# Performance work log

Measured on AMD Instinct MI355X. Metric: run time of the kernel, lower is better.

The kernel has to match this reference:

```python
import jax, jax.numpy as jnp
import numpy as np

# Hyperparameters from init_kwargs
K = 1024           # num_embeddings
D = 256            # embedding_dim
COMMIT = 0.25      # commitment_cost
DECAY = 0.99
LAMBDA = 1e-05
NU = 0.1
TAU = 0.5


def setup_inputs() -> dict:
    key = jax.random.key(0)
    k1, k2, k3 = jax.random.split(key, 3)
    B, H, W = 32, 32, 32
    N = B * H * W
    inputs = jax.random.normal(k1, (B, D, H, W), jnp.float32)
    weight = jax.random.normal(k2, (K, D), jnp.float32) * 0.02  # codebook
    # EMA buffers as initialized on first training step (non-kmeans branch)
    ema_count = jnp.full((K,), N / K, jnp.float32)
    ema_weight = weight * ema_count[:, None]
    # Gumbel noise used by F.gumbel_softmax(-distances, tau, hard=True)
    gumbel_noise = jax.random.gumbel(k3, (N, K), jnp.float32)
    return {"inputs": inputs, "weight": weight, "ema_count": ema_count,
            "ema_weight": ema_weight, "gumbel_noise": gumbel_noise}


def reference(inputs, weight, ema_count, ema_weight, gumbel_noise):
    B, C, H, W = inputs.shape
    # b d h w -> (b h w) d
    x = jnp.transpose(inputs, (0, 2, 3, 1)).reshape(-1, C)  # [N, D]
    N = x.shape[0]

    distances = (jnp.sum(x * x, axis=1, keepdims=True)
                 + jnp.sum(weight * weight, axis=1)
                 - 2.0 * jnp.einsum('nd,kd->nk', x, weight))

    soft_encodings = jax.nn.softmax(-distances / TAU, axis=-1)  # [N, K]

    # Hard gumbel-softmax sample (computed under no_grad in torch):
    # argmax((logits + g)/tau) == argmax(logits + g), logits = -distances
    idx = jnp.argmax(-distances + gumbel_noise, axis=-1)        # [N]
    encodings = jax.nn.one_hot(idx, K, dtype=x.dtype)           # [N, K]

    quantized = (encodings @ weight).reshape(B, H, W, C)        # [B,H,W,D]

    # EMA codebook update (training branch, no_grad)
    new_count = ema_count * DECAY + jnp.sum(soft_encodings, axis=0) * (1.0 - DECAY)
    new_count = (new_count + LAMBDA) / (N + K * LAMBDA) * N
    d_weight = jnp.einsum('nk,nd->kd', soft_encodings, x)
    new_ema_weight = ema_weight * DECAY + d_weight * (1.0 - DECAY)
    new_embedding = new_ema_weight / new_count[:, None]

    # Negative-entropy commitment loss on soft assignments
    probs = soft_encodings
    loss_latents = jnp.mean(jnp.sum(probs * jnp.log(jnp.clip(probs, 1e-08)), axis=-1))
    loss = COMMIT * loss_latents

    # quantized + nu*(quantized - detach(quantized)) == quantized in value
    quantized = quantized + NU * (quantized - jax.lax.stop_gradient(quantized))

    avg_probs = jnp.mean(encodings, axis=0)
    perplexity = jnp.exp(-jnp.sum(avg_probs * jnp.log(avg_probs + 1e-10)))

    quantized_out = jnp.transpose(quantized, (0, 3, 1, 2))  # [B,D,H,W]
    return (loss, quantized_out, perplexity, encodings,
            new_count, new_ema_weight, new_embedding)
```

## Files before the change

kernel.cpp:

```cpp
#include <hip/hip_runtime.h>
#include <math.h>

#define NROWS 32768
#define KCB   1024
#define DDIM  256
#define NHALF 16384

#define O_LOSS 0
#define O_Q    1
#define O_PERP 8388609
#define O_ENC  8388610
#define O_NCNT 41943042
#define O_EMAW 41944066
#define O_EMB  42206210

#define E_XS3   2
#define E_S     12582914

#define W_WSQ  0
#define W_XSQ  1024
#define W_IDX  33792
#define W_COL  66560
#define W_HCNT 67584
#define W_BENT 68608
#define W_NCNT 76800
#define W_T2I  77824
#define W_WB   143360
#define W_MROW 274432
#define W_IROW 307200

typedef __attribute__((ext_vector_type(8))) short bf16x8;
typedef __attribute__((ext_vector_type(4))) float f32x4;

#define GLOAD_LDS16(g, l) __builtin_amdgcn_global_load_lds( \
    (const __attribute__((address_space(1))) unsigned int*)(g), \
    (__attribute__((address_space(3))) unsigned int*)(l), 16, 0, 0)

__device__ __forceinline__ float wred_sum(float v) {
#pragma unroll
  for (int off = 32; off > 0; off >>= 1) v += __shfl_xor(v, off);
  return v;
}
__device__ __forceinline__ ushort f2bf(float f) {
  union { float f; unsigned u; } c; c.f = f;
  unsigned u = c.u;
  return (ushort)((u + 0x7fffu + ((u >> 16) & 1u)) >> 16);
}
__device__ __forceinline__ float bf2f(ushort h) {
  union { unsigned u; float f; } c; c.u = ((unsigned)h) << 16;
  return c.f;
}

__global__ void k_init(float* __restrict__ hcnt) {
  int i = blockIdx.x * 256 + threadIdx.x;
  if (i < 1024) hcnt[i] = 0.f;
}

__global__ void k_wsplit(const float* __restrict__ w, float* __restrict__ wsq,
                         ushort* __restrict__ WB) {
  int t = threadIdx.x;
  int lane = t & 63, wv = t >> 6;
  int k = blockIdx.x * 4 + wv;
  int d0 = lane * 4;
  float4 v = *(const float4*)&w[(size_t)k * DDIM + d0];
  float s = v.x * v.x + v.y * v.y + v.z * v.z + v.w * v.w;
  s = wred_sum(s);
  if (lane == 0) wsq[k] = s;
  float vv[4] = {v.x, v.y, v.z, v.w};
  union { ushort u[4]; uint2 q; } hh;
#pragma unroll
  for (int q = 0; q < 4; ++q) hh.u[q] = f2bf(vv[q]);
  *(uint2*)&WB[(size_t)k * 256 + d0] = hh.q;
}

__global__ __launch_bounds__(256) void k_xsplit(const float* __restrict__ x,
                                                ushort* __restrict__ XS3,
                                                float* __restrict__ xsq) {
  __shared__ __align__(16) ushort sl[32 * 776];
  __shared__ float sq[32 * 9];
  int t = threadIdx.x;
  int b = blockIdx.x >> 5, mt = blockIdx.x & 31;
  int m0 = mt * 32, mloc = t & 31, dgrp = t >> 5;
  const float* xb = x + (size_t)b * DDIM * 1024 + m0 + mloc;
  float s = 0.f;
#pragma unroll
  for (int jj = 0; jj < 8; ++jj) {
    int d0 = dgrp * 32 + jj * 4;
    float vv[4];
#pragma unroll
    for (int q = 0; q < 4; ++q) vv[q] = xb[(size_t)(d0 + q) * 1024];
    union { ushort u[4]; uint2 q; } hh, mi, lo;
#pragma unroll
    for (int q = 0; q < 4; ++q) {
      float v = vv[q];
      ushort h = f2bf(v);
      float r1 = v - bf2f(h);
      ushort m_ = f2bf(r1);
      float r2 = r1 - bf2f(m_);
      hh.u[q] = h; mi.u[q] = m_; lo.u[q] = f2bf(r2);
      s = fmaf(v, v, s);
    }
    int base = mloc * 776;
    *(uint2*)&sl[base + d0] = hh.q;
    *(uint2*)&sl[base + 256 + d0] = mi.q;
    *(uint2*)&sl[base + 512 + d0] = lo.q;
  }
  sq[mloc * 9 + dgrp] = s;
  __syncthreads();
  if (t < 32) {
    float ss = 0.f;
#pragma unroll
    for (int gq = 0; gq < 8; ++gq) ss += sq[t * 9 + gq];
    xsq[b * 1024 + m0 + t] = ss;
  }
  ushort* dst = XS3 + (size_t)(b * 1024 + m0) * 768;
#pragma unroll
  for (int p = 0; p < 12; ++p) {
    int idx = p * 256 + t;
    int row = idx / 96;
    int co = idx - row * 96;
    *(uint4*)&dst[(size_t)row * 768 + co * 8] = *(uint4*)&sl[row * 776 + co * 8];
  }
}

__global__ __launch_bounds__(256) void k_gemm1t(const ushort* __restrict__ XS3h,
                                                const ushort* __restrict__ WB,
                                                const float* __restrict__ wsq,
                                                const float* __restrict__ xsqh,
                                                float* __restrict__ S) {
  __shared__ __align__(16) ushort Asl[2][8192];
  __shared__ __align__(16) ushort Bsl[2][8192];
  __shared__ float xsl[128];
  __shared__ float wsl[128];
  int t = threadIdx.x;
  int h = blockIdx.x;
  int xcd = h & 7, seq = h >> 3;
  int kt = seq & 7;
  int nt = xcd * 16 + (seq >> 3);
  int n0 = nt * 128;
  int k0 = kt * 128;
  int l = t & 63, wid = t >> 6;
  int wr = wid >> 1, wc = wid & 1;
  int hi = l >> 4, c = l & 15;

  if (t < 128) { xsl[t] = xsqh[n0 + t]; wsl[t] = wsq[k0 + t]; }

  f32x4 zero = {0.f, 0.f, 0.f, 0.f};
  f32x4 acc[4][4];
#pragma unroll
  for (int i = 0; i < 4; ++i)
#pragma unroll
    for (int j = 0; j < 4; ++j) acc[i][j] = zero;

  const char* XSb = (const char*)XS3h;
  const char* WBb = (const char*)WB;
  int lr = l >> 3;
  int lsw = ((l & 7) ^ lr) << 4;

#define STAGE(s_, b_)                                                              \
  {                                                                                \
    size_t bofs_ = (size_t)((s_) & 3) << 7;                                        \
    size_t aofs_ = ((s_) < 4) ? ((size_t)(s_) << 7)                                \
                              : (size_t)(512 + (((s_) - 4) << 7));                 \
    char* Ad_ = (char*)Asl + (b_) * 16384;                                         \
    char* Bd_ = (char*)Bsl + (b_) * 16384;                                         \
    _Pragma("unroll")                                                              \
    for (int q_ = 0; q_ < 4; ++q_) {                                               \
      int seg_ = wid * 32 + q_ * 8;                                                \
      GLOAD_LDS16(XSb + (size_t)(n0 + seg_ + lr) * 1536 + aofs_ + lsw,             \
                  Ad_ + seg_ * 128);                                               \
      GLOAD_LDS16(WBb + (size_t)(k0 + seg_ + lr) * 512 + bofs_ + lsw,              \
                  Bd_ + seg_ * 128);                                               \
    }                                                                              \
  }

  STAGE(0, 0);
  asm volatile("s_waitcnt vmcnt(0)" ::: "memory");
  __builtin_amdgcn_s_barrier();
  __builtin_amdgcn_sched_barrier(0);

  int buf = 0;
  for (int s = 0; s < 8; ++s) {
    if (s < 7) STAGE(s + 1, buf ^ 1);
    const ushort* Ab = &Asl[buf][0];
    const ushort* Bb = &Bsl[buf][0];
#pragma unroll
    for (int kk = 0; kk < 2; ++kk) {
      bf16x8 af[4], bg[4];
#pragma unroll
      for (int i = 0; i < 4; ++i) {
        int row = wr * 64 + i * 16 + c;
        int ch = (kk * 4 + hi) ^ (row & 7);
        af[i] = *(const bf16x8*)&Ab[row * 64 + ch * 8];
      }
#pragma unroll
      for (int j = 0; j < 4; ++j) {
        int row = wc * 64 + j * 16 + c;
        int ch = (kk * 4 + hi) ^ (row & 7);
        bg[j] = *(const bf16x8*)&Bb[row * 64 + ch * 8];
      }
#pragma unroll
      for (int i = 0; i < 4; ++i)
#pragma unroll
        for (int j = 0; j < 4; ++j)
          acc[i][j] = __builtin_amdgcn_mfma_f32_16x16x32_bf16(af[i], bg[j], acc[i][j], 0, 0, 0);
    }
    asm volatile("s_waitcnt vmcnt(0)" ::: "memory");
    __builtin_amdgcn_s_barrier();
    buf ^= 1;
  }
#undef STAGE

#pragma unroll
  for (int i = 0; i < 4; ++i) {
#pragma unroll
    for (int r = 0; r < 4; ++r) {
      int nl = wr * 64 + i * 16 + hi * 4 + r;
      float xs = xsl[nl];
#pragma unroll
      for (int j = 0; j < 4; ++j) {
        int kl = wc * 64 + j * 16 + c;
        float nd = fmaf(2.f, acc[i][j][r], -(xs + wsl[kl]));
        S[(size_t)(n0 + nl) * 1024 + k0 + kl] = nd;
      }
    }
  }
}

__global__ __launch_bounds__(256) void k_rowstat(const float* __restrict__ S,
                                                 const float* __restrict__ Gh,
                                                 float* __restrict__ Mrowh,
                                                 float* __restrict__ Irowh,
                                                 float* __restrict__ benth,
                                                 int* __restrict__ t2igh) {
  __shared__ float went[4];
  int t = threadIdx.x;
  int l = t & 63, wv = t >> 6;
  int n = blockIdx.x * 4 + wv;
  const float* row = S + ((size_t)n << 10);
  const float* grow = Gh + ((size_t)n << 10);
  float v[16];
  float mx = -3.0e38f;
  float v1 = -3.0e38f, v2 = -3.0e38f;
  int i1 = 0x7fffffff, i2 = 0x7fffffff;
#pragma unroll
  for (int j = 0; j < 4; ++j) {
    float4 a = *(const float4*)&row[j * 256 + l * 4];
    float4 gg = *(const float4*)&grow[j * 256 + l * 4];
    float av[4] = {a.x, a.y, a.z, a.w};
    float gv[4] = {gg.x, gg.y, gg.z, gg.w};
#pragma unroll
    for (int q = 0; q < 4; ++q) {
      v[j * 4 + q] = av[q];
      mx = fmaxf(mx, av[q]);
      float sc = av[q] + gv[q];
      int kk = j * 256 + l * 4 + q;
      if (sc > v1 || (sc == v1 && kk < i1)) { v2 = v1; i2 = i1; v1 = sc; i1 = kk; }
      else if (sc > v2 || (sc == v2 && kk < i2)) { v2 = sc; i2 = kk; }
    }
  }
#pragma unroll
  for (int off = 1; off < 64; off <<= 1) {
    mx = fmaxf(mx, __shfl_xor(mx, off));
    float ov1 = __shfl_xor(v1, off), ov2 = __shfl_xor(v2, off);
    int oi1 = __shfl_xor(i1, off), oi2 = __shfl_xor(i2, off);
    bool fB = (ov1 > v1) || (ov1 == v1 && oi1 < i1);
    float nv1 = fB ? ov1 : v1; int ni1 = fB ? oi1 : i1;
    float ca = fB ? v1 : ov1;  int cia = fB ? i1 : oi1;
    float cb = fB ? ov2 : v2;  int cib = fB ? oi2 : i2;
    bool sB = (cb > ca) || (cb == ca && cib < cia);
    v1 = nv1; i1 = ni1;
    v2 = sB ? cb : ca; i2 = sB ? cib : cia;
  }
  float M = 2.f * mx;
  float e[16]; float ps = 0.f;
#pragma unroll
  for (int u = 0; u < 16; ++u) { e[u] = __expf(fmaf(2.f, v[u], -M)); ps += e[u]; }
  ps = wred_sum(ps);
  float inv = 1.f / ps;
  float ent = 0.f;
#pragma unroll
  for (int u = 0; u < 16; ++u) {
    float sfv = e[u] * inv;
    ent += sfv * __logf(fmaxf(sfv, 1e-8f));
  }
  ent = wred_sum(ent);
  if (l == 0) {
    t2igh[n * 2] = i1; t2igh[n * 2 + 1] = i2;
    Mrowh[n] = M; Irowh[n] = inv;
    went[wv] = ent;
  }
  __syncthreads();
  if (t == 0) benth[blockIdx.x] = went[0] + went[1] + went[2] + went[3];
}

__global__ __launch_bounds__(512) void k_rowwrite(const float* __restrict__ S,
                                                  const float* __restrict__ Mrowh,
                                                  const float* __restrict__ Irowh,
                                                  ushort* __restrict__ sTp) {
  __shared__ ushort lds[64 * 65];
  __shared__ float Ml[64], Il[64];
  int t = threadIdx.x;
  int n0 = blockIdx.x * 64;
  if (t < 64) { Ml[t] = Mrowh[n0 + t]; Il[t] = Irowh[n0 + t]; }
  __syncthreads();
  for (int kt = 0; kt < 16; ++kt) {
    int k0 = kt * 64;
    int row = t >> 3, c8 = (t & 7) * 8;
    float M = Ml[row], inv = Il[row];
    const float* sp = &S[(size_t)(n0 + row) * 1024 + k0 + c8];
    float4 a = *(const float4*)sp;
    float4 b = *(const float4*)(sp + 4);
    float sv[8] = {a.x, a.y, a.z, a.w, b.x, b.y, b.z, b.w};
    ushort* d = &lds[row * 65 + c8];
#pragma unroll
    for (int j = 0; j < 8; ++j)
      d[j] = f2bf(__expf(fmaf(2.f, sv[j], -M)) * inv);
    __syncthreads();
    int krow = t >> 3, nc8 = (t & 7) * 8;
    uint* dst = (uint*)&sTp[(size_t)(k0 + krow) * NHALF + n0 + nc8];
#pragma unroll
    for (int j = 0; j < 4; ++j) {
      uint lo = lds[(nc8 + 2 * j) * 65 + krow];
      uint hh = lds[(nc8 + 2 * j + 1) * 65 + krow];
      dst[j] = lo | (hh << 16);
    }
    __syncthreads();
  }
}

__global__ __launch_bounds__(256) void k_refine(const ushort* __restrict__ XS3,
                                                const float* __restrict__ w,
                                                const float* __restrict__ wsq,
                                                const float* __restrict__ xsq,
                                                const float* __restrict__ G,
                                                const int* __restrict__ t2ig,
                                                int* __restrict__ idxArr,
                                                float* __restrict__ hcnt) {
  int t = threadIdx.x;
  int l = t & 63, wv = t >> 6;
  int base = blockIdx.x * 64 + wv * 16;
  int d0 = l * 4;
  for (int rr = 0; rr < 16; ++rr) {
    int n = base + rr;
    const ushort* p = XS3 + (size_t)n * 768;
    union { uint2 q; ushort u[4]; } ha, ma, la;
    ha.q = *(const uint2*)&p[d0];
    ma.q = *(const uint2*)&p[256 + d0];
    la.q = *(const uint2*)&p[512 + d0];
    float xv[4];
#pragma unroll
    for (int q = 0; q < 4; ++q) xv[q] = bf2f(ha.u[q]) + bf2f(ma.u[q]) + bf2f(la.u[q]);
    float xs = xsq[n];
    int ia = t2ig[n * 2], ib = t2ig[n * 2 + 1];
    float sc[2];
    int ids[2] = {ia, ib};
#pragma unroll
    for (int cdd = 0; cdd < 2; ++cdd) {
      int id = ids[cdd];
      const float* wr = w + (size_t)id * DDIM;
      float4 wv4 = *(const float4*)&wr[d0];
      float d = xv[0] * wv4.x + xv[1] * wv4.y + xv[2] * wv4.z + xv[3] * wv4.w;
      d = wred_sum(d);
      sc[cdd] = fmaf(2.f, d, -xs) - wsq[id] + G[((size_t)n << 10) + id];
    }
    int win = (sc[1] > sc[0] || (sc[1] == sc[0] && ib < ia)) ? ib : ia;
    if (l == 0) {
      idxArr[n] = win;
      atomicAdd(&hcnt[win], 1.f);
    }
  }
}

__global__ void k_quant(const float* __restrict__ w, const int* __restrict__ idxArr,
                        float* __restrict__ outQ) {
  int n = blockIdx.x * 256 + threadIdx.x;
  int b = n >> 10, m = n & 1023;
  int id = idxArr[n];
  const float* wr = w + (size_t)id * DDIM;
  float* o = outQ + (size_t)b * DDIM * 1024 + m;
#pragma unroll 4
  for (int d = 0; d < DDIM; ++d) o[(size_t)d * 1024] = wr[d];
}

__global__ __launch_bounds__(512) void k_gemm2_mfma(const ushort* __restrict__ sT0,
                                                    const ushort* __restrict__ sT1,
                                                    const float* __restrict__ x,
                                                    float* __restrict__ P) {
  __shared__ __align__(16) ushort Abuf[256 * 72];
  __shared__ __align__(16) ushort Bbuf[128 * 72];
  int t = threadIdx.x;
  int h = blockIdx.x;
  int xcd = h & 7, seq = h >> 3;
  int ns = xcd * 4 + (seq >> 3);
  int ktdt = seq & 7;
  int kt = ktdt & 3, dt = ktdt >> 2;
  int k0 = kt * 256, d0 = dt * 128;
  int l = t & 63, wv = t >> 6;
  int wk = wv >> 1, wd = wv & 1;
  const ushort* Abase = (ns < 16) ? sT0 : sT1;
  size_t nloc0 = (size_t)(ns & 15) * 1024;
  f32x4 zero = {0.f, 0.f, 0.f, 0.f};
  f32x4 acc[4][4];
#pragma unroll
  for (int i = 0; i < 4; ++i)
#pragma unroll
    for (int j = 0; j < 4; ++j) acc[i][j] = zero;

  int colv = (t & 7) * 8;
  int rbase = t >> 3;
  for (int s = 0; s < 16; ++s) {
#pragma unroll
    for (int p = 0; p < 4; ++p) {
      int row = p * 64 + rbase;
      const uint* ap = (const uint*)(Abase + (size_t)(k0 + row) * NHALF + nloc0 + s * 64 + colv);
      uint4 v; v.x = ap[0]; v.y = ap[1]; v.z = ap[2]; v.w = ap[3];
      *(uint4*)&Abuf[row * 72 + colv] = v;
    }
#pragma unroll
    for (int p = 0; p < 2; ++p) {
      int row = p * 64 + rbase;
      const float* xp = &x[((size_t)ns * DDIM + d0 + row) * 1024 + s * 64 + colv];
      float4 a = *(const float4*)xp;
      float4 b = *(const float4*)(xp + 4);
      union { ushort u[8]; uint4 q; } pk;
      pk.u[0] = f2bf(a.x); pk.u[1] = f2bf(a.y); pk.u[2] = f2bf(a.z); pk.u[3] = f2bf(a.w);
      pk.u[4] = f2bf(b.x); pk.u[5] = f2bf(b.y); pk.u[6] = f2bf(b.z); pk.u[7] = f2bf(b.w);
      *(uint4*)&Bbuf[row * 72 + colv] = pk.q;
    }
    __syncthreads();
    bf16x8 af[4], bfr[4];
#pragma unroll
    for (int nb2 = 0; nb2 < 2; ++nb2) {
#pragma unroll
      for (int sub = 0; sub < 4; ++sub) {
        af[sub] = *(const bf16x8*)&Abuf[(wk * 64 + sub * 16 + (l & 15)) * 72 + nb2 * 32 + (l >> 4) * 8];
        bfr[sub] = *(const bf16x8*)&Bbuf[(wd * 64 + sub * 16 + (l & 15)) * 72 + nb2 * 32 + (l >> 4) * 8];
      }
#pragma unroll
      for (int i = 0; i < 4; ++i)
#pragma unroll
        for (int j = 0; j < 4; ++j)
          acc[i][j] = __builtin_amdgcn_mfma_f32_16x16x32_bf16(af[i], bfr[j], acc[i][j], 0, 0, 0);
    }
    __syncthreads();
  }
  float* Pb = P + (size_t)ns * (KCB * DDIM);
#pragma unroll
  for (int i = 0; i < 4; ++i)
#pragma unroll
    for (int j = 0; j < 4; ++j) {
#pragma unroll
      for (int r = 0; r < 4; ++r) {
        int k = k0 + wk * 64 + i * 16 + (l >> 4) * 4 + r;
        int d = d0 + wd * 64 + j * 16 + (l & 15);
        Pb[(size_t)k * DDIM + d] = acc[i][j][r];
      }
    }
}

__global__ void k_colsum2(const ushort* __restrict__ sT0, const ushort* __restrict__ sT1,
                          float* __restrict__ colsum) {
  int k = blockIdx.x;
  int t = threadIdx.x;
  const uint* r0 = (const uint*)(sT0 + (size_t)k * NHALF);
  const uint* r1 = (const uint*)(sT1 + (size_t)k * NHALF);
  float s = 0.f;
#pragma unroll
  for (int cc = 0; cc < 8; ++cc) {
#pragma unroll
    for (int q = 0; q < 4; ++q) {
      uint a = r0[cc * 1024 + t * 4 + q];
      uint b = r1[cc * 1024 + t * 4 + q];
      s += bf2f((ushort)(a & 0xffffu)) + bf2f((ushort)(a >> 16));
      s += bf2f((ushort)(b & 0xffffu)) + bf2f((ushort)(b >> 16));
    }
  }
  s = wred_sum(s);
  __shared__ float ws4[4];
  if ((t & 63) == 0) ws4[t >> 6] = s;
  __syncthreads();
  if (t == 0) colsum[k] = ws4[0] + ws4[1] + ws4[2] + ws4[3];
}

__global__ void k_final1(const float* __restrict__ ema_count, const float* __restrict__ colsum,
                         const float* __restrict__ hcnt, const float* __restrict__ bent,
                         float* __restrict__ ncnt, float* __restrict__ out) {
  __shared__ float red[1024];
  int t = threadIdx.x;
  const float onem = 1.0f - 0.99f;
  float nc = ema_count[t] * 0.99f + colsum[t] * onem;
  nc = (nc + 1e-5f) / (32768.0f + 1024.0f * 1e-5f) * 32768.0f;
  out[O_NCNT + t] = nc;
  ncnt[t] = nc;
  float s = 0.f;
  for (int i = t; i < 8192; i += 1024) s += bent[i];
  red[t] = s;
  __syncthreads();
  for (int off = 512; off > 0; off >>= 1) { if (t < off) red[t] += red[t + off]; __syncthreads(); }
  if (t == 0) out[O_LOSS] = 0.25f * (red[0] / 32768.0f);
  __syncthreads();
  float avg = hcnt[t] * (1.0f / 32768.0f);
  red[t] = avg * logf(avg + 1e-10f);
  __syncthreads();
  for (int off = 512; off > 0; off >>= 1) { if (t < off) red[t] += red[t + off]; __syncthreads(); }
  if (t == 0) out[O_PERP] = expf(-red[0]);
}

__global__ void k_reduce_final2(const float* __restrict__ P, const float* __restrict__ ema_w,
                                const float* __restrict__ ncnt, float* __restrict__ outEW,
                                float* __restrict__ outEMB) {
  int i = blockIdx.x * 256 + threadIdx.x;
  float s = 0.f;
#pragma unroll
  for (int ns = 0; ns < 32; ++ns) s += P[(size_t)ns * (KCB * DDIM) + i];
  float ew = ema_w[i] * 0.99f + s * 0.01f;
  outEW[i] = ew;
  outEMB[i] = ew / ncnt[i >> 8];
}

__global__ void k_onehot(const int* __restrict__ idxArr, float* __restrict__ E) {
  int gid = blockIdx.x * 256 + threadIdx.x;
  int n = gid >> 8;
  int k4 = (gid & 255) * 4;
  int id = idxArr[n];
  float2* E2 = (float2*)E;
  size_t base = ((size_t)n * KCB + k4) >> 1;
  float2 vA = {(float)(k4 == id), (float)(k4 + 1 == id)};
  float2 vB = {(float)(k4 + 2 == id), (float)(k4 + 3 == id)};
  E2[base] = vA;
  E2[base + 1] = vB;
}

extern "C" void kernel_launch(void* const* d_in, const int* in_sizes, int n_in,
                              void* d_out, int out_size, void* d_ws, size_t ws_size,
                              hipStream_t stream) {
  const float* x = (const float*)d_in[0];
  const float* w = (const float*)d_in[1];
  const float* ema_count = (const float*)d_in[2];
  const float* ema_w = (const float*)d_in[3];
  const float* g = (const float*)d_in[4];
  float* out = (float*)d_out;
  float* ws = (float*)d_ws;

  float* wsq    = ws + W_WSQ;
  float* xsq    = ws + W_XSQ;
  int*   idxArr = (int*)(ws + W_IDX);
  float* colsum = ws + W_COL;
  float* hcnt   = ws + W_HCNT;
  float* bent   = ws + W_BENT;
  float* ncnt   = ws + W_NCNT;
  int*   top2i  = (int*)(ws + W_T2I);
  ushort* WB    = (ushort*)(ws + W_WB);
  float* Mrow   = ws + W_MROW;
  float* Irow   = ws + W_IROW;

  float* outQ = out + O_Q;
  float* outE = out + O_ENC;

  ushort* XS3    = (ushort*)(outE + E_XS3);
  float*  Sslot  = outE + E_S;
  ushort* softT1 = (ushort*)(outE + E_XS3);
  ushort* softT0 = (ushort*)outQ;

  k_init<<<4, 256, 0, stream>>>(hcnt);
  k_wsplit<<<256, 256, 0, stream>>>(w, wsq, WB);
  k_xsplit<<<1024, 256, 0, stream>>>(x, XS3, xsq);
  k_gemm1t<<<1024, 256, 0, stream>>>(XS3, WB, wsq, xsq, Sslot);
  k_rowstat<<<4096, 256, 0, stream>>>(Sslot, g, Mrow, Irow, bent, top2i);
  k_rowwrite<<<256, 512, 0, stream>>>(Sslot, Mrow, Irow, softT0);
  k_gemm1t<<<1024, 256, 0, stream>>>(XS3 + (size_t)NHALF * 768, WB,
                                     wsq, xsq + NHALF, Sslot);
  k_rowstat<<<4096, 256, 0, stream>>>(Sslot, g + (size_t)NHALF * 1024,
                                      Mrow + NHALF, Irow + NHALF,
                                      bent + 4096, top2i + NHALF * 2);
  k_refine<<<512, 256, 0, stream>>>(XS3, w, wsq, xsq, g, top2i, idxArr, hcnt);
  k_rowwrite<<<256, 512, 0, stream>>>(Sslot, Mrow + NHALF, Irow + NHALF, softT1);
  k_colsum2<<<1024, 256, 0, stream>>>(softT0, softT1, colsum);
  k_gemm2_mfma<<<256, 512, 0, stream>>>(softT0, softT1, x, Sslot);
  k_final1<<<1, 1024, 0, stream>>>(ema_count, colsum, hcnt, bent, ncnt, out);
  k_reduce_final2<<<1024, 256, 0, stream>>>(Sslot, ema_w, ncnt, out + O_EMAW, out + O_EMB);
  k_quant<<<128, 256, 0, stream>>>(w, idxArr, outQ);
  k_onehot<<<32768, 256, 0, stream>>>(idxArr, outE);
}
```

Measured before the change: 330.9 us.

## Fuse first-half rowstat with rowwrite and fold colsum into gemm2

For the first half of the rows, row statistics (max, top-2 Gumbel, entropy) and the transposed bf16 softmax write are merged into one kernel, so the score matrix is read from L2/HBM once instead of twice. The separate column-sum kernel is dropped. Column sums are now accumulated from the A fragments already loaded inside the MFMA gemm2 and added with atomics. This saves kernel launches and a full pass over the soft-encoding matrix, but the atomic adds make the column sums order-nondeterministic, and the entropy partial-sum layout changes to 256 + 4096 entries.

Result: no change. 333.3 us (median of 2 runs) (+0.7%).

```diff
diff --git a/kernel.cpp b/kernel.cpp
--- a/kernel.cpp
+++ b/kernel.cpp
@@ -51,9 +51,9 @@
   return c.f;
 }
 
-__global__ void k_init(float* __restrict__ hcnt) {
+__global__ void k_init(float* __restrict__ hcnt, float* __restrict__ colsum) {
   int i = blockIdx.x * 256 + threadIdx.x;
-  if (i < 1024) hcnt[i] = 0.f;
+  if (i < 1024) { hcnt[i] = 0.f; colsum[i] = 0.f; }
 }
 
 __global__ void k_wsplit(const float* __restrict__ w, float* __restrict__ wsq,
@@ -227,6 +227,108 @@
   }
 }
 
+__global__ __launch_bounds__(512) void k_rowfuse(const float* __restrict__ S,
+                                                 const float* __restrict__ Gh,
+                                                 float* __restrict__ benth,
+                                                 int* __restrict__ t2igh,
+                                                 ushort* __restrict__ sTp) {
+  __shared__ ushort lds[64 * 65];
+  __shared__ float Ml[64], Il[64];
+  __shared__ float went[8];
+  int t = threadIdx.x;
+  int l = t & 63, wv = t >> 6;
+  int n0 = blockIdx.x * 64;
+  float entacc = 0.f;
+  for (int it = 0; it < 8; ++it) {
+    int nloc = wv * 8 + it;
+    int n = n0 + nloc;
+    const float* row = S + ((size_t)n << 10);
+    const float* grow = Gh + ((size_t)n << 10);
+    float v[16];
+    float mx = -3.0e38f;
+    float v1 = -3.0e38f, v2 = -3.0e38f;
+    int i1 = 0x7fffffff, i2 = 0x7fffffff;
+#pragma unroll
+    for (int j = 0; j < 4; ++j) {
+      float4 a = *(const float4*)&row[j * 256 + l * 4];
+      float4 gg = *(const float4*)&grow[j * 256 + l * 4];
+      float av[4] = {a.x, a.y, a.z, a.w};
+      float gv[4] = {gg.x, gg.y, gg.z, gg.w};
+#pragma unroll
+      for (int q = 0; q < 4; ++q) {
+        v[j * 4 + q] = av[q];
+        mx = fmaxf(mx, av[q]);
+        float sc = av[q] + gv[q];
+        int kk = j * 256 + l * 4 + q;
+        if (sc > v1 || (sc == v1 && kk < i1)) { v2 = v1; i2 = i1; v1 = sc; i1 = kk; }
+        else if (sc > v2 || (sc == v2 && kk < i2)) { v2 = sc; i2 = kk; }
+      }
+    }
+#pragma unroll
+    for (int off = 1; off < 64; off <<= 1) {
+      mx = fmaxf(mx, __shfl_xor(mx, off));
+      float ov1 = __shfl_xor(v1, off), ov2 = __shfl_xor(v2, off);
+      int oi1 = __shfl_xor(i1, off), oi2 = __shfl_xor(i2, off);
+      bool fB = (ov1 > v1) || (ov1 == v1 && oi1 < i1);
+      float nv1 = fB ? ov1 : v1; int ni1 = fB ? oi1 : i1;
+      float ca = fB ? v1 : ov1;  int cia = fB ? i1 : oi1;
+      float cb = fB ? ov2 : v2;  int cib = fB ? oi2 : i2;
+      bool sB = (cb > ca) || (cb == ca && cib < cia);
+      v1 = nv1; i1 = ni1;
+      v2 = sB ? cb : ca; i2 = sB ? cib : cia;
+    }
+    float M = 2.f * mx;
+    float e[16]; float ps = 0.f;
+#pragma unroll
+    for (int u = 0; u < 16; ++u) { e[u] = __expf(fmaf(2.f, v[u], -M)); ps += e[u]; }
+    ps = wred_sum(ps);
+    float inv = 1.f / ps;
+    float ent = 0.f;
+#pragma unroll
+    for (int u = 0; u < 16; ++u) {
+      float sfv = e[u] * inv;
+      ent += sfv * __logf(fmaxf(sfv, 1e-8f));
+    }
+    ent = wred_sum(ent);
+    entacc += ent;
+    if (l == 0) {
+      t2igh[n * 2] = i1; t2igh[n * 2 + 1] = i2;
+      Ml[nloc] = M; Il[nloc] = inv;
+    }
+  }
+  if (l == 0) went[wv] = entacc;
+  __syncthreads();
+  if (t == 0) {
+    float s = 0.f;
+#pragma unroll
+    for (int q = 0; q < 8; ++q) s += went[q];
+    benth[blockIdx.x] = s;
+  }
+  int row2 = t >> 3, c8 = (t & 7) * 8;
+  float M2 = Ml[row2], inv2 = Il[row2];
+  for (int kt = 0; kt < 16; ++kt) {
+    int k0 = kt * 64;
+    const float* sp = &S[(size_t)(n0 + row2) * 1024 + k0 + c8];
+    float4 a = *(const float4*)sp;
+    float4 b = *(const float4*)(sp + 4);
+    float sv[8] = {a.x, a.y, a.z, a.w, b.x, b.y, b.z, b.w};
+    ushort* d = &lds[row2 * 65 + c8];
+#pragma unroll
+    for (int j = 0; j < 8; ++j)
+      d[j] = f2bf(__expf(fmaf(2.f, sv[j], -M2)) * inv2);
+    __syncthreads();
+    int krow = t >> 3, nc8 = (t & 7) * 8;
+    uint* dst = (uint*)&sTp[(size_t)(k0 + krow) * NHALF + n0 + nc8];
+#pragma unroll
+    for (int j = 0; j < 4; ++j) {
+      uint lo = lds[(nc8 + 2 * j) * 65 + krow];
+      uint hh = lds[(nc8 + 2 * j + 1) * 65 + krow];
+      dst[j] = lo | (hh << 16);
+    }
+    __syncthreads();
+  }
+}
+
 __global__ __launch_bounds__(256) void k_rowstat(const float* __restrict__ S,
                                                  const float* __restrict__ Gh,
                                                  float* __restrict__ Mrowh,
@@ -386,7 +488,8 @@
 __global__ __launch_bounds__(512) void k_gemm2_mfma(const ushort* __restrict__ sT0,
                                                     const ushort* __restrict__ sT1,
                                                     const float* __restrict__ x,
-                                                    float* __restrict__ P) {
+                                                    float* __restrict__ P,
+                                                    float* __restrict__ colsum) {
   __shared__ __align__(16) ushort Abuf[256 * 72];
   __shared__ __align__(16) ushort Bbuf[128 * 72];
   int t = threadIdx.x;
@@ -406,6 +509,7 @@
   for (int i = 0; i < 4; ++i)
 #pragma unroll
     for (int j = 0; j < 4; ++j) acc[i][j] = zero;
+  float colacc[4] = {0.f, 0.f, 0.f, 0.f};
 
   int colv = (t & 7) * 8;
   int rbase = t >> 3;
@@ -437,6 +541,13 @@
         af[sub] = *(const bf16x8*)&Abuf[(wk * 64 + sub * 16 + (l & 15)) * 72 + nb2 * 32 + (l >> 4) * 8];
         bfr[sub] = *(const bf16x8*)&Bbuf[(wd * 64 + sub * 16 + (l & 15)) * 72 + nb2 * 32 + (l >> 4) * 8];
       }
+      if (dt == 0 && wd == 0) {
+#pragma unroll
+        for (int sub = 0; sub < 4; ++sub)
+#pragma unroll
+          for (int q = 0; q < 8; ++q)
+            colacc[sub] += bf2f((ushort)af[sub][q]);
+      }
 #pragma unroll
       for (int i = 0; i < 4; ++i)
 #pragma unroll
@@ -457,30 +568,15 @@
         Pb[(size_t)k * DDIM + d] = acc[i][j][r];
       }
     }
-}
-
-__global__ void k_colsum2(const ushort* __restrict__ sT0, const ushort* __restrict__ sT1,
-                          float* __restrict__ colsum) {
-  int k = blockIdx.x;
-  int t = threadIdx.x;
-  const uint* r0 = (const uint*)(sT0 + (size_t)k * NHALF);
-  const uint* r1 = (const uint*)(sT1 + (size_t)k * NHALF);
-  float s = 0.f;
-#pragma unroll
-  for (int cc = 0; cc < 8; ++cc) {
-#pragma unroll
-    for (int q = 0; q < 4; ++q) {
-      uint a = r0[cc * 1024 + t * 4 + q];
-      uint b = r1[cc * 1024 + t * 4 + q];
-      s += bf2f((ushort)(a & 0xffffu)) + bf2f((ushort)(a >> 16));
-      s += bf2f((ushort)(b & 0xffffu)) + bf2f((ushort)(b >> 16));
-    }
-  }
-  s = wred_sum(s);
-  __shared__ float ws4[4];
-  if ((t & 63) == 0) ws4[t >> 6] = s;
-  __syncthreads();
-  if (t == 0) colsum[k] = ws4[0] + ws4[1] + ws4[2] + ws4[3];
+  if (dt == 0 && wd == 0) {
+#pragma unroll
+    for (int sub = 0; sub < 4; ++sub) {
+      float s = colacc[sub];
+      s += __shfl_xor(s, 16);
+      s += __shfl_xor(s, 32);
+      if (l < 16) atomicAdd(&colsum[k0 + wk * 64 + sub * 16 + l], s);
+    }
+  }
 }
 
 __global__ void k_final1(const float* __restrict__ ema_count, const float* __restrict__ colsum,
@@ -494,7 +590,7 @@
   out[O_NCNT + t] = nc;
   ncnt[t] = nc;
   float s = 0.f;
-  for (int i = t; i < 8192; i += 1024) s += bent[i];
+  for (int i = t; i < 4352; i += 1024) s += bent[i];
   red[t] = s;
   __syncthreads();
   for (int off = 512; off > 0; off >>= 1) { if (t < off) red[t] += red[t + off]; __syncthreads(); }
@@ -563,21 +659,18 @@
   ushort* softT1 = (ushort*)(outE + E_XS3);
   ushort* softT0 = (ushort*)outQ;
 
-  k_init<<<4, 256, 0, stream>>>(hcnt);
+  k_init<<<4, 256, 0, stream>>>(hcnt, colsum);
   k_wsplit<<<256, 256, 0, stream>>>(w, wsq, WB);
   k_xsplit<<<1024, 256, 0, stream>>>(x, XS3, xsq);
   k_gemm1t<<<1024, 256, 0, stream>>>(XS3, WB, wsq, xsq, Sslot);
-  k_rowstat<<<4096, 256, 0, stream>>>(Sslot, g, Mrow, Irow, bent, top2i);
-  k_rowwrite<<<256, 512, 0, stream>>>(Sslot, Mrow, Irow, softT0);
+  k_rowfuse<<<256, 512, 0, stream>>>(Sslot, g, bent, top2i, softT0);
   k_gemm1t<<<1024, 256, 0, stream>>>(XS3 + (size_t)NHALF * 768, WB,
                                      wsq, xsq + NHALF, Sslot);
   k_rowstat<<<4096, 256, 0, stream>>>(Sslot, g + (size_t)NHALF * 1024,
-                                      Mrow + NHALF, Irow + NHALF,
-                                      bent + 4096, top2i + NHALF * 2);
+                                      Mrow, Irow, bent + 256, top2i + NHALF * 2);
   k_refine<<<512, 256, 0, stream>>>(XS3, w, wsq, xsq, g, top2i, idxArr, hcnt);
-  k_rowwrite<<<256, 512, 0, stream>>>(Sslot, Mrow + NHALF, Irow + NHALF, softT1);
-  k_colsum2<<<1024, 256, 0, stream>>>(softT0, softT1, colsum);
-  k_gemm2_mfma<<<256, 512, 0, stream>>>(softT0, softT1, x, Sslot);
+  k_rowwrite<<<256, 512, 0, stream>>>(Sslot, Mrow, Irow, softT1);
+  k_gemm2_mfma<<<256, 512, 0, stream>>>(softT0, softT1, x, Sslot, colsum);
   k_final1<<<1, 1024, 0, stream>>>(ema_count, colsum, hcnt, bent, ncnt, out);
   k_reduce_final2<<<1024, 256, 0, stream>>>(Sslot, ema_w, ncnt, out + O_EMAW, out + O_EMB);
   k_quant<<<128, 256, 0, stream>>>(w, idxArr, outQ);
```
